# Kernel tuning notes

Hardware: AMD Instinct MI355X
Metric: run time of the kernel (lower is better)

## Reference

```python
import jax, jax.numpy as jnp
import numpy as np

N_NODES = 50000
N_GRAPHS = 64
LRELU_SLOPE = 0.2
BN_EPS = 1e-5

def _conv1d(x, w, b):
    # x: [B, C_in, L], w: [C_out, C_in, K] -> [B, C_out, L-K+1]
    y = jax.lax.conv_general_dilated(x, w, window_strides=(1,), padding='VALID',
                                     dimension_numbers=('NCH', 'OIH', 'NCH'))
    return y + b[None, :, None]

def setup_inputs() -> dict:
    key = jax.random.key(0)
    ks = jax.random.split(key, 24)
    E = 800000
    inp = {
        'global_rna': jax.random.randint(ks[0], (64, 3000), 0, 5, dtype=jnp.int32),
        'local_rna': jax.random.randint(ks[1], (64, 2998), 0, 65, dtype=jnp.int32),
        'pro_x': jax.random.normal(ks[2], (N_NODES, 33), jnp.float32),
        'edge_index': jax.random.randint(ks[3], (2, E), 0, N_NODES, dtype=jnp.int32),
        'pro_weight': jax.random.uniform(ks[4], (E,), jnp.float32),
        'pro_batch': jnp.sort(jax.random.randint(ks[5], (N_NODES,), 0, N_GRAPHS, dtype=jnp.int32)),
        'emb1': jax.random.normal(ks[6], (5, 128), jnp.float32),
        'emb2': jax.random.normal(ks[7], (65, 128), jnp.float32),
        'conv1_w': jax.random.normal(ks[8], (32, 3000, 8), jnp.float32) * 0.02,
        'conv1_b': jax.random.normal(ks[9], (32,), jnp.float32) * 0.02,
        'conv2_w': jax.random.normal(ks[10], (32, 2998, 8), jnp.float32) * 0.02,
        'conv2_b': jax.random.normal(ks[11], (32,), jnp.float32) * 0.02,
        'fc_xr_w': jax.random.normal(ks[12], (128, 3872), jnp.float32) * 0.02,
        'fc_xr_b': jax.random.normal(ks[13], (128,), jnp.float32) * 0.02,
        'gcn_w': jax.random.normal(ks[14], (33, 33), jnp.float32) * 0.1,
        'gcn_b': jax.random.normal(ks[15], (33,), jnp.float32) * 0.1,
        'bn_mean': jnp.zeros((33,), jnp.float32),
        'bn_var': jnp.ones((33,), jnp.float32),
        'bn_weight': jnp.ones((33,), jnp.float32),
        'bn_bias': jnp.zeros((33,), jnp.float32),
        'gat_wl': jax.random.normal(ks[16], (132, 33), jnp.float32) * 0.1,
        'gat_wr': jax.random.normal(ks[17], (132, 33), jnp.float32) * 0.1,
        'gat_att': jax.random.normal(ks[18], (2, 66), jnp.float32) * 0.1,
        'gat_b': jax.random.normal(ks[19], (132,), jnp.float32) * 0.1,
        'fc1_w': jax.random.normal(ks[20], (1024, 132), jnp.float32) * 0.05,
        'fc1_b': jax.random.normal(ks[21], (1024,), jnp.float32) * 0.05,
        'fc2_w': jax.random.normal(ks[22], (128, 1024), jnp.float32) * 0.05,
        'fc2_b': jax.random.normal(ks[23], (128,), jnp.float32) * 0.05,
    }
    return inp

def _forward(global_rna, local_rna, pro_x, edge_index, pro_weight, pro_batch,
             emb1, emb2, conv1_w, conv1_b, conv2_w, conv2_b, fc_xr_w, fc_xr_b,
             gcn_w, gcn_b, bn_mean, bn_var, bn_weight, bn_bias,
             gat_wl, gat_wr, gat_att, gat_b, fc1_w, fc1_b, fc2_w, fc2_b):
    # ---- RNA global branch ----
    xrg = emb1[global_rna]                       # [B, 3000, 128]
    xrg = _conv1d(xrg, conv1_w, conv1_b)         # [B, 32, 121]
    xrg = xrg.reshape(-1, 32 * 121) @ fc_xr_w.T + fc_xr_b
    # ---- RNA local branch ----
    xrl = emb2[local_rna]                        # [B, 2998, 128]
    xrl = _conv1d(xrl, conv2_w, conv2_b)         # [B, 32, 121]
    xrl = xrl.reshape(-1, 32 * 121) @ fc_xr_w.T + fc_xr_b
    # ---- protein GCNConv (with self-loops, symmetric norm, edge weights) ----
    N = pro_x.shape[0]
    loop = jnp.arange(N, dtype=edge_index.dtype)
    src = jnp.concatenate([edge_index[0], loop])
    dst = jnp.concatenate([edge_index[1], loop])
    w = jnp.concatenate([pro_weight, jnp.ones((N,), pro_weight.dtype)])
    deg = jax.ops.segment_sum(w, dst, num_segments=N)
    dinv = jnp.where(deg > 0, jax.lax.rsqrt(deg), 0.0)
    norm = dinv[src] * w * dinv[dst]
    h = pro_x @ gcn_w.T                          # [N, 33]
    xp = jax.ops.segment_sum(h[src] * norm[:, None], dst, num_segments=N) + gcn_b
    xp = jax.nn.relu(xp)
    # ---- NodeLevelBatchNorm (eval: running stats) ----
    inv = bn_weight * jax.lax.rsqrt(bn_var + BN_EPS)
    xp = xp * inv + (bn_bias - bn_mean * inv)
    # ---- GATv2Conv (heads=2, out=66, concat, self-loops, eval: no dropout) ----
    H, C = 2, 66
    xl = (xp @ gat_wl.T).reshape(N, H, C)
    xr = (xp @ gat_wr.T).reshape(N, H, C)
    e = jnp.sum(jax.nn.leaky_relu(xl[src] + xr[dst], LRELU_SLOPE) * gat_att, axis=-1)  # [E2, H]
    emax = jax.ops.segment_max(e, dst, num_segments=N)                                  # [N, H]
    a = jnp.exp(e - emax[dst])
    asum = jax.ops.segment_sum(a, dst, num_segments=N)
    alpha = a / asum[dst]                                                              # [E2, H]
    xp = jax.ops.segment_sum(xl[src] * alpha[:, :, None], dst, num_segments=N)
    xp = xp.reshape(N, H * C) + gat_b
    xp = jax.nn.relu(xp)
    # ---- global mean pool ----
    cnt = jax.ops.segment_sum(jnp.ones((N,), xp.dtype), pro_batch, num_segments=N_GRAPHS)
    xp = jax.ops.segment_sum(xp, pro_batch, num_segments=N_GRAPHS) / jnp.maximum(cnt, 1.0)[:, None]
    # ---- protein MLP head (dropout = identity in eval) ----
    xp = jax.nn.relu(xp @ fc1_w.T + fc1_b)
    xp = xp @ fc2_w.T + fc2_b
    xc_rna = 0.5 * (xrg + xrl)
    return (xc_rna, xp)

def reference(global_rna, local_rna, pro_x, edge_index, pro_weight, pro_batch,
              emb1, emb2, conv1_w, conv1_b, conv2_w, conv2_b, fc_xr_w, fc_xr_b,
              gcn_w, gcn_b, bn_mean, bn_var, bn_weight, bn_bias,
              gat_wl, gat_wr, gat_att, gat_b, fc1_w, fc1_b, fc2_w, fc2_b):
    return _forward(global_rna, local_rna, pro_x, edge_index, pro_weight, pro_batch,
                    emb1, emb2, conv1_w, conv1_b, conv2_w, conv2_b, fc_xr_w, fc_xr_b,
                    gcn_w, gcn_b, bn_mean, bn_var, bn_weight, bn_bias,
                    gat_wl, gat_wr, gat_att, gat_b, fc1_w, fc1_b, fc2_w, fc2_b)
```

## Files before the change

### kernel.cpp

```cpp
#include <hip/hip_runtime.h>

#define N_NODES 50000
#define N_EDGES 800000
#define LRELU_SLOPE 0.2f
#define BN_EPS 1e-5f

typedef unsigned int u32;
typedef unsigned long long u64;

__device__ __forceinline__ float lrelu(float x){ return fmaxf(x,0.f) + LRELU_SLOPE*fminf(x,0.f); }
__device__ __forceinline__ float bflo(u32 u){ return __uint_as_float(u<<16); }
__device__ __forceinline__ float bfhi(u32 u){ return __uint_as_float(u & 0xffff0000u); }
__device__ __forceinline__ u32 packbf(float a, float b){
  u32 ua = __float_as_uint(a); ua = (ua + 0x7fffu + ((ua>>16)&1u)) >> 16;
  u32 ub = __float_as_uint(b); ub = (ub + 0x7fffu + ((ub>>16)&1u)) >> 16;
  return ua | (ub<<16);
}
__device__ __forceinline__ float degof(u64 p){
  return (float)(p & 0xFFFFFFFFFFull) * (1.0f/67108864.0f);
}

__global__ __launch_bounds__(256) void k_hist(const int* __restrict__ eidx, const float* __restrict__ pw,
                                              u64* __restrict__ pk){
  int e = blockIdx.x*256 + threadIdx.x;
  if(e < N_EDGES){
    int d = eidx[N_EDGES + e];
    u64 q = (u64)(pw[e] * 67108864.f);
    atomicAdd(&pk[d], (1ull<<40) | q);
  }
}

__global__ __launch_bounds__(256) void k_scan1(const u64* __restrict__ pk, int* __restrict__ rowptr,
                                               int* __restrict__ bsum){
  __shared__ int sc[256];
  int b = blockIdx.x, t = threadIdx.x;
  int i = b*256 + t;
  int v = (i < N_NODES) ? (int)(pk[i] >> 40) : 0;
  sc[t] = v;
  __syncthreads();
  for(int off=1; off<256; off<<=1){
    int x = (t>=off)? sc[t-off] : 0;
    __syncthreads();
    sc[t] += x;
    __syncthreads();
  }
  if(i < N_NODES) rowptr[i] = sc[t] - v;
  if(t == 255) bsum[b] = sc[255];
}

__global__ __launch_bounds__(256) void k_scan2(const int* __restrict__ bsum, int* __restrict__ bbase,
                                               int* __restrict__ rowptr, int* __restrict__ gstart,
                                               int* __restrict__ gend){
  __shared__ int sc[256];
  int t = threadIdx.x;
  int v = (t < 196) ? bsum[t] : 0;
  sc[t] = v;
  __syncthreads();
  for(int off=1; off<256; off<<=1){
    int x = (t>=off)? sc[t-off] : 0;
    __syncthreads();
    sc[t] += x;
    __syncthreads();
  }
  if(t < 196) bbase[t] = sc[t] - v;
  if(t == 255) rowptr[N_NODES] = sc[255];
  if(t < 64){ gstart[t] = N_NODES; gend[t] = 0; }
}

__global__ __launch_bounds__(256) void k_scan3(int* __restrict__ rowptr, const int* __restrict__ bbase){
  int b = blockIdx.x, t = threadIdx.x;
  int i = b*256 + t;
  if(i < N_NODES) rowptr[i] += bbase[b];
}

__global__ __launch_bounds__(256) void k_scatter(const int* __restrict__ eidx, const float* __restrict__ pw,
                                                 const int* __restrict__ rowptr, int* __restrict__ fill,
                                                 const u64* __restrict__ pk, uint2* __restrict__ s_srcw){
  int e = blockIdx.x*256 + threadIdx.x;
  if(e < N_EDGES){
    int d = eidx[N_EDGES + e];
    int s = eidx[e];
    float ge = rsqrtf(degof(pk[s]) + 1.f) * pw[e];
    int pos = rowptr[d] + atomicAdd(&fill[d], 1);
    uint2 pr; pr.x = (u32)s; pr.y = __float_as_uint(ge);
    s_srcw[pos] = pr;
  }
}

__global__ __launch_bounds__(256) void k_h(const float* __restrict__ px, const float* __restrict__ gw,
                                           u32* __restrict__ hb){
  int n = blockIdx.x*256 + threadIdx.x;
  if(n >= N_NODES) return;
  float x[33];
  #pragma unroll
  for(int k=0;k<33;k++) x[k] = px[n*33+k];
  float a[33];
  for(int c=0;c<33;c++){
    float s = 0.f;
    #pragma unroll
    for(int k=0;k<33;k++) s = fmaf(x[k], gw[c*33+k], s);
    a[c] = s;
  }
  #pragma unroll
  for(int d=0;d<16;d++) hb[(size_t)n*17 + d] = packbf(a[2*d], a[2*d+1]);
  hb[(size_t)n*17 + 16] = packbf(a[32], 0.f);
}

__global__ __launch_bounds__(256) void k_gcn(const u32* __restrict__ hb, const int* __restrict__ rowptr,
                                             const uint2* __restrict__ s_srcw,
                                             const u64* __restrict__ pk,
                                             const float* __restrict__ gcnb, const float* __restrict__ bnm,
                                             const float* __restrict__ bnv, const float* __restrict__ bnw,
                                             const float* __restrict__ bnb, float* __restrict__ xp1){
  int wave = threadIdx.x >> 6;
  int lane = threadIdx.x & 63;
  int n = blockIdx.x*4 + wave;
  if(n >= N_NODES) return;
  int l = lane & 15, g = lane >> 4;
  bool t0 = (l == 0);
  float dn = rsqrtf(degof(pk[n]) + 1.f);
  const u32* srow = hb + (size_t)n*17;
  u32 us  = srow[l];
  u32 ust = t0 ? srow[16] : 0u;
  float acc0, acc1, acct;
  if(g == 0){ acc0 = dn*bflo(us); acc1 = dn*bfhi(us); acct = dn*bflo(ust); }
  else      { acc0 = 0.f; acc1 = 0.f; acct = 0.f; }
  int rb = rowptr[n], re = rowptr[n+1];
  int j = rb;
  for(; j+8 <= re; j += 8){
    uint2 prA = s_srcw[j + g];
    uint2 prB = s_srcw[j + 4 + g];
    float geA = __uint_as_float(prA.y);
    float geB = __uint_as_float(prB.y);
    const u32* rA = hb + (size_t)prA.x*17;
    const u32* rB = hb + (size_t)prB.x*17;
    u32 uA  = rA[l], uB = rB[l];
    u32 utA = t0 ? rA[16] : 0u;
    u32 utB = t0 ? rB[16] : 0u;
    acc0 = fmaf(geA, bflo(uA),  fmaf(geB, bflo(uB),  acc0));
    acc1 = fmaf(geA, bfhi(uA),  fmaf(geB, bfhi(uB),  acc1));
    acct = fmaf(geA, bflo(utA), fmaf(geB, bflo(utB), acct));
  }
  if(j+4 <= re){
    uint2 pr = s_srcw[j + g];
    float ge = __uint_as_float(pr.y);
    const u32* r = hb + (size_t)pr.x*17;
    u32 u  = r[l];
    u32 ut = t0 ? r[16] : 0u;
    acc0 = fmaf(ge, bflo(u),  acc0);
    acc1 = fmaf(ge, bfhi(u),  acc1);
    acct = fmaf(ge, bflo(ut), acct);
    j += 4;
  }
  int rem = re - j;
  if(rem > 0){
    bool val = (g < rem);
    uint2 pr = s_srcw[val ? (j + g) : j];
    float ge = val ? __uint_as_float(pr.y) : 0.f;
    const u32* r = hb + (size_t)pr.x*17;
    u32 u  = r[l];
    u32 ut = t0 ? r[16] : 0u;
    acc0 = fmaf(ge, bflo(u),  acc0);
    acc1 = fmaf(ge, bfhi(u),  acc1);
    acct = fmaf(ge, bflo(ut), acct);
  }
  #pragma unroll
  for(int m=16;m<=32;m<<=1){
    acc0 += __shfl_xor(acc0, m, 64);
    acc1 += __shfl_xor(acc1, m, 64);
    acct += __shfl_xor(acct, m, 64);
  }
  if(g == 0){
    int c0 = 2*l, c1 = 2*l+1;
    float v0 = fmaxf(dn*acc0 + gcnb[c0], 0.f);
    float v1 = fmaxf(dn*acc1 + gcnb[c1], 0.f);
    float i0 = bnw[c0] / sqrtf(bnv[c0] + BN_EPS);
    float i1 = bnw[c1] / sqrtf(bnv[c1] + BN_EPS);
    float2 o;
    o.x = v0*i0 + (bnb[c0] - bnm[c0]*i0);
    o.y = v1*i1 + (bnb[c1] - bnm[c1]*i1);
    ((float2*)(xp1 + (size_t)n*36))[l] = o;
    if(t0){
      float vt = fmaxf(dn*acct + gcnb[32], 0.f);
      float it = bnw[32] / sqrtf(bnv[32] + BN_EPS);
      float2 ot; ot.x = vt*it + (bnb[32] - bnm[32]*it); ot.y = 0.f;
      ((float2*)(xp1 + (size_t)n*36))[16] = ot;
      float2 z; z.x = 0.f; z.y = 0.f;
      ((float2*)(xp1 + (size_t)n*36))[17] = z;
    }
  }
}

__global__ __launch_bounds__(320) void k_gatlin(const float* __restrict__ xp1, const float* __restrict__ wl,
                                                const float* __restrict__ wr, u32* __restrict__ xlb,
                                                float* __restrict__ xr){
  __shared__ float sx[64*36];
  __shared__ float swle[66*33];
  __shared__ float swlo[66*33];
  __shared__ float swre[66*33];
  __shared__ float swro[66*33];
  int t = threadIdx.x;
  int n0 = blockIdx.x*64;
  int nn = N_NODES - n0; if(nn > 64) nn = 64;
  for(int i=t;i<2178;i+=320){
    int d = i/33, k = i - d*33;
    int gb = d*66 + k;
    swle[i] = wl[gb];
    swlo[i] = wl[gb+33];
    swre[i] = wr[gb];
    swro[i] = wr[gb+33];
  }
  int xcnt = nn*36;
  for(int i=t;i<xcnt;i+=320) sx[i] = xp1[(size_t)n0*36 + i];
  __syncthreads();
  if(t >= 264) return;
  int ng = t/66, p = t - ng*66;
  int nbase = ng*16;
  float al0[16], al1[16], ar0[16], ar1[16];
  #pragma unroll
  for(int i=0;i<16;i++){ al0[i]=0.f; al1[i]=0.f; ar0[i]=0.f; ar1[i]=0.f; }
  const float* wle = swle + p*33;
  const float* wlo = swlo + p*33;
  const float* wre = swre + p*33;
  const float* wro = swro + p*33;
  for(int k=0;k<33;k++){
    float w0 = wle[k], w1 = wlo[k], w2 = wre[k], w3 = wro[k];
    const float* xcol = sx + nbase*36 + k;
    #pragma unroll
    for(int i=0;i<16;i++){
      float x = xcol[i*36];
      al0[i] = fmaf(x, w0, al0[i]);
      al1[i] = fmaf(x, w1, al1[i]);
      ar0[i] = fmaf(x, w2, ar0[i]);
      ar1[i] = fmaf(x, w3, ar1[i]);
    }
  }
  int head = (p >= 33) ? 1 : 0;
  int dd = p - 33*head;
  #pragma unroll
  for(int i=0;i<16;i++){
    int n = nbase + i;
    if(n < nn){
      size_t nidx = (size_t)(n0 + n);
      xlb[nidx*68 + head*34 + dd] = packbf(al0[i], al1[i]);
      float2 v; v.x = ar0[i]; v.y = ar1[i];
      ((float2*)xr)[nidx*66 + p] = v;
    }
  }
}

__global__ __launch_bounds__(128) void k_gat(const int* __restrict__ rowptr, const u32* __restrict__ srcx,
                                             const u32* __restrict__ xlb, const float* __restrict__ xr,
                                             const float* __restrict__ att, const float* __restrict__ gatb,
                                             float* __restrict__ xp2){
  int n = blockIdx.x;
  int h = threadIdx.x >> 6;
  int lane = threadIdx.x & 63;
  int l = lane & 15, g = lane >> 4;
  int base = h*66, dbase = h*34;
  bool t0 = (l == 0);
  size_t nrow = (size_t)n*132;
  const float2* xr2 = (const float2*)(xr + nrow + base);
  float2 xra = xr2[2*l], xrb = xr2[2*l+1];
  float2 xrt = t0 ? xr2[32] : make_float2(0.f,0.f);
  const float2* att2 = (const float2*)(att + base);
  float2 ata = att2[2*l], atb = att2[2*l+1];
  float2 att_t = att2[32];
  const u32* srow = xlb + (size_t)n*68 + dbase;
  uint2 su = ((const uint2*)srow)[l];
  u32 ust = t0 ? srow[32] : 0u;
  float s0 = bflo(su.x), s1 = bfhi(su.x), s2 = bflo(su.y), s3 = bfhi(su.y);
  float st0 = bflo(ust), st1 = bfhi(ust);
  float p = lrelu(s0+xra.x)*ata.x + lrelu(s1+xra.y)*ata.y
          + lrelu(s2+xrb.x)*atb.x + lrelu(s3+xrb.y)*atb.y
          + lrelu(st0+xrt.x)*att_t.x + lrelu(st1+xrt.y)*att_t.y;
  #pragma unroll
  for(int m=1;m<=8;m<<=1) p += __shfl_xor(p, m, 64);
  float e_self = p;
  float a0_, a1_, a2_, a3_, at0, at1, asum;
  if(g == 0){ a0_=s0; a1_=s1; a2_=s2; a3_=s3; at0=st0; at1=st1; asum=1.f; }
  else      { a0_=0.f; a1_=0.f; a2_=0.f; a3_=0.f; at0=0.f; at1=0.f; asum=0.f; }
  int rb = rowptr[n], re = rowptr[n+1];
  int j = rb;
  for(; j+8 <= re; j += 8){
    int sA = (int)srcx[2*(j + g)];
    int sB = (int)srcx[2*(j + 4 + g)];
    const u32* rA = xlb + (size_t)sA*68 + dbase;
    const u32* rB = xlb + (size_t)sB*68 + dbase;
    uint2 uA = ((const uint2*)rA)[l];
    uint2 uB = ((const uint2*)rB)[l];
    u32 utA = t0 ? rA[32] : 0u;
    u32 utB = t0 ? rB[32] : 0u;
    float vA0=bflo(uA.x), vA1=bfhi(uA.x), vA2=bflo(uA.y), vA3=bfhi(uA.y);
    float vB0=bflo(uB.x), vB1=bfhi(uB.x), vB2=bflo(uB.y), vB3=bfhi(uB.y);
    float wA0=bflo(utA), wA1=bfhi(utA);
    float wB0=bflo(utB), wB1=bfhi(utB);
    float pA = lrelu(vA0+xra.x)*ata.x + lrelu(vA1+xra.y)*ata.y
             + lrelu(vA2+xrb.x)*atb.x + lrelu(vA3+xrb.y)*atb.y
             + lrelu(wA0+xrt.x)*att_t.x + lrelu(wA1+xrt.y)*att_t.y;
    float pB = lrelu(vB0+xra.x)*ata.x + lrelu(vB1+xra.y)*ata.y
             + lrelu(vB2+xrb.x)*atb.x + lrelu(vB3+xrb.y)*atb.y
             + lrelu(wB0+xrt.x)*att_t.x + lrelu(wB1+xrt.y)*att_t.y;
    #pragma unroll
    for(int m=1;m<=8;m<<=1){
      pA += __shfl_xor(pA, m, 64);
      pB += __shfl_xor(pB, m, 64);
    }
    float aA = __expf(pA - e_self);
    float aB = __expf(pB - e_self);
    a0_ = fmaf(aA, vA0, fmaf(aB, vB0, a0_));
    a1_ = fmaf(aA, vA1, fmaf(aB, vB1, a1_));
    a2_ = fmaf(aA, vA2, fmaf(aB, vB2, a2_));
    a3_ = fmaf(aA, vA3, fmaf(aB, vB3, a3_));
    at0 = fmaf(aA, wA0, fmaf(aB, wB0, at0));
    at1 = fmaf(aA, wA1, fmaf(aB, wB1, at1));
    asum += aA + aB;
  }
  if(j+4 <= re){
    int s = (int)srcx[2*(j + g)];
    const u32* r = xlb + (size_t)s*68 + dbase;
    uint2 uu = ((const uint2*)r)[l];
    u32 ut = t0 ? r[32] : 0u;
    float v0=bflo(uu.x), v1=bfhi(uu.x), v2=bflo(uu.y), v3=bfhi(uu.y);
    float w0=bflo(ut), w1=bfhi(ut);
    float pp = lrelu(v0+xra.x)*ata.x + lrelu(v1+xra.y)*ata.y
             + lrelu(v2+xrb.x)*atb.x + lrelu(v3+xrb.y)*atb.y
             + lrelu(w0+xrt.x)*att_t.x + lrelu(w1+xrt.y)*att_t.y;
    #pragma unroll
    for(int m=1;m<=8;m<<=1) pp += __shfl_xor(pp, m, 64);
    float a = __expf(pp - e_self);
    a0_ = fmaf(a, v0, a0_); a1_ = fmaf(a, v1, a1_);
    a2_ = fmaf(a, v2, a2_); a3_ = fmaf(a, v3, a3_);
    at0 = fmaf(a, w0, at0); at1 = fmaf(a, w1, at1);
    asum += a;
    j += 4;
  }
  int rem = re - j;
  if(rem > 0){
    bool val = (g < rem);
    int s = val ? (int)srcx[2*(j + g)] : n;
    const u32* r = xlb + (size_t)s*68 + dbase;
    uint2 uu = ((const uint2*)r)[l];
    u32 ut = t0 ? r[32] : 0u;
    float v0=bflo(uu.x), v1=bfhi(uu.x), v2=bflo(uu.y), v3=bfhi(uu.y);
    float w0=bflo(ut), w1=bfhi(ut);
    float pp = lrelu(v0+xra.x)*ata.x + lrelu(v1+xra.y)*ata.y
             + lrelu(v2+xrb.x)*atb.x + lrelu(v3+xrb.y)*atb.y
             + lrelu(w0+xrt.x)*att_t.x + lrelu(w1+xrt.y)*att_t.y;
    #pragma unroll
    for(int m=1;m<=8;m<<=1) pp += __shfl_xor(pp, m, 64);
    float a = val ? __expf(pp - e_self) : 0.f;
    a0_ = fmaf(a, v0, a0_); a1_ = fmaf(a, v1, a1_);
    a2_ = fmaf(a, v2, a2_); a3_ = fmaf(a, v3, a3_);
    at0 = fmaf(a, w0, at0); at1 = fmaf(a, w1, at1);
    asum += a;
  }
  #pragma unroll
  for(int m=16;m<=32;m<<=1){
    a0_ += __shfl_xor(a0_, m, 64);
    a1_ += __shfl_xor(a1_, m, 64);
    a2_ += __shfl_xor(a2_, m, 64);
    a3_ += __shfl_xor(a3_, m, 64);
    at0 += __shfl_xor(at0, m, 64);
    at1 += __shfl_xor(at1, m, 64);
    asum += __shfl_xor(asum, m, 64);
  }
  float inv = 1.f/asum;
  if(g == 0){
    const float2* gb2 = (const float2*)(gatb + base);
    float2 ga = gb2[2*l], gb = gb2[2*l+1];
    float2* o2 = (float2*)(xp2 + nrow + base);
    float2 oa, ob;
    oa.x = fmaxf(a0_*inv + ga.x, 0.f); oa.y = fmaxf(a1_*inv + ga.y, 0.f);
    ob.x = fmaxf(a2_*inv + gb.x, 0.f); ob.y = fmaxf(a3_*inv + gb.y, 0.f);
    o2[2*l] = oa; o2[2*l+1] = ob;
    if(t0){
      float2 gt = gb2[32];
      float2 ot;
      ot.x = fmaxf(at0*inv + gt.x, 0.f); ot.y = fmaxf(at1*inv + gt.y, 0.f);
      o2[32] = ot;
    }
  }
}

__global__ __launch_bounds__(256) void k_bounds(const int* __restrict__ batch, int* __restrict__ gstart,
                                                int* __restrict__ gend){
  int n = blockIdx.x*256 + threadIdx.x;
  if(n >= N_NODES) return;
  int b = batch[n];
  if(n == 0) gstart[b] = 0;
  else {
    int p = batch[n-1];
    if(p != b){ gstart[b] = n; gend[p] = n; }
  }
  if(n == N_NODES-1) gend[b] = N_NODES;
}

__global__ __launch_bounds__(128) void k_poolp(const float* __restrict__ xp2, const int* __restrict__ gstart,
                                               const int* __restrict__ gend, float* __restrict__ pp){
  int g = blockIdx.x, seg = blockIdx.y, t = threadIdx.x;
  int s = gstart[g], e = gend[g];
  int len = e - s; if(len < 0) len = 0;
  int ns = s + (int)(((long long)len*seg)>>4);
  int ne = s + (int)(((long long)len*(seg+1))>>4);
  float a0 = 0.f, a1 = 0.f;
  for(int n=ns;n<ne;n++){
    a0 += xp2[(size_t)n*132 + t];
    if(t < 4) a1 += xp2[(size_t)n*132 + 128 + t];
  }
  float* o = pp + (size_t)(g*16 + seg)*132;
  o[t] = a0;
  if(t < 4) o[128 + t] = a1;
}

__global__ __launch_bounds__(256) void k_pfc1(const float* __restrict__ pp, const int* __restrict__ gstart,
                                              const int* __restrict__ gend, const float* __restrict__ w,
                                              const float* __restrict__ b, float* __restrict__ h1T){
  __shared__ float pooled[132];
  int g = blockIdx.x, t = threadIdx.x;
  if(t < 132){
    float s = 0.f;
    #pragma unroll
    for(int k=0;k<16;k++) s += pp[(size_t)(g*16 + k)*132 + t];
    int c = gend[g] - gstart[g]; if(c < 1) c = 1;
    pooled[t] = s/(float)c;
  }
  __syncthreads();
  #pragma unroll
  for(int r=0;r<4;r++){
    int o = r*256 + t;
    const float* wr = w + o*132;
    float acc = b[o];
    for(int k=0;k<132;k++) acc = fmaf(pooled[k], wr[k], acc);
    h1T[o*64+g] = fmaxf(acc, 0.f);
  }
}

__global__ __launch_bounds__(256) void k_fc2(const float* __restrict__ h1T, const float* __restrict__ w,
                                             const float* __restrict__ b, float* __restrict__ out){
  __shared__ float part[256];
  int o = blockIdx.x, t = threadIdx.x;
  int s = t >> 6, g = t & 63;
  const float* wr = w + o*1024 + s*256;
  const float* hp = h1T + (size_t)(s*256)*64 + g;
  float acc = 0.f;
  for(int k=0;k<256;k++) acc = fmaf(hp[k*64], wr[k], acc);
  part[t] = acc;
  __syncthreads();
  if(s == 0){
    float r = b[o] + part[g] + part[64+g] + part[128+g] + part[192+g];
    out[8192 + g*128 + o] = r;
  }
}

__global__ __launch_bounds__(256) void k_bucket(const int* __restrict__ g, int L, int V,
                                                int* __restrict__ sci, int* __restrict__ off){
  __shared__ int gl[3000];
  __shared__ int hist[65];
  __shared__ int base[66];
  int b = blockIdx.x, t = threadIdx.x;
  if(t < V) hist[t] = 0;
  for(int i=t;i<L;i+=256) gl[i] = g[b*L + i];
  __syncthreads();
  for(int i=t;i<L;i+=256) atomicAdd(&hist[gl[i]], 1);
  __syncthreads();
  if(t == 0){
    int run = 0;
    for(int v=0;v<V;v++){ base[v] = run; run += hist[v]; }
    base[V] = run;
  }
  __syncthreads();
  if(t <= V) off[b*(V+1) + t] = base[t];
  if(t < V) hist[t] = 0;
  __syncthreads();
  for(int i=t;i<L;i+=256){
    int v = gl[i];
    int p = base[v] + atomicAdd(&hist[v], 1);
    sci[b*3000 + p] = i*8;
  }
}

__global__ __launch_bounds__(256) void k_sgather(const int* __restrict__ sci, const int* __restrict__ off,
                                                 const float* __restrict__ w, int V, int wstride,
                                                 int sstride, float* __restrict__ S){
  __shared__ int loff[66];
  __shared__ int lci[3000];
  int b = blockIdx.x, q = blockIdx.y, t = threadIdx.x;
  int nsplit = gridDim.y;
  if(t <= V) loff[t] = off[b*(V+1) + t];
  __syncthreads();
  int vs = (V*q)/nsplit, ve = (V*(q+1))/nsplit;
  if(vs == ve) return;
  int p0 = loff[vs], p1 = loff[ve];
  for(int i=p0+t;i<p1;i+=256) lci[i-p0] = sci[b*3000 + i];
  __syncthreads();
  int co = t >> 3, kk = t & 7;
  const float* wrow = w + co*wstride + kk;
  float* Srow = S + (size_t)b*32*sstride + co*sstride + kk;
  for(int v=vs;v<ve;v++){
    int j = loff[v] - p0, je = loff[v+1] - p0;
    float a0=0.f,a1=0.f,a2=0.f,a3=0.f,a4=0.f,a5=0.f,a6=0.f,a7=0.f;
    for(; j+8 <= je; j += 8){
      a0 += wrow[lci[j]];
      a1 += wrow[lci[j+1]];
      a2 += wrow[lci[j+2]];
      a3 += wrow[lci[j+3]];
      a4 += wrow[lci[j+4]];
      a5 += wrow[lci[j+5]];
      a6 += wrow[lci[j+6]];
      a7 += wrow[lci[j+7]];
    }
    for(; j<je; j++) a0 += wrow[lci[j]];
    Srow[v*8] = ((a0+a1)+(a2+a3)) + ((a4+a5)+(a6+a7));
  }
}

__global__ __launch_bounds__(128) void k_y(const float* __restrict__ S1, const float* __restrict__ S2,
                                           const float* __restrict__ emb1, const float* __restrict__ emb2,
                                           const float* __restrict__ c1b, const float* __restrict__ c2b,
                                           float* __restrict__ ysum){
  __shared__ float em1[640];
  __shared__ float em2[8320];
  __shared__ float Sa[320];
  __shared__ float Sb[4160];
  int b = blockIdx.x, cg = blockIdx.y, t = threadIdx.x;
  for(int i=t;i<640;i+=128)  em1[i] = emb1[i];
  for(int i=t;i<8320;i+=128) em2[i] = emb2[i];
  for(int i=t;i<320;i+=128)  Sa[i] = S1[b*1280 + cg*320 + i];
  for(int i=t;i<4160;i+=128) Sb[i] = S2[(size_t)b*16640 + cg*4160 + i];
  __syncthreads();
  if(t >= 121) return;
  #pragma unroll
  for(int c8=0;c8<8;c8++){
    int co = cg*8 + c8;
    const float* sa = Sa + c8*40;
    float acc1 = c1b[co];
    #pragma unroll
    for(int v=0;v<5;v++)
      #pragma unroll
      for(int k=0;k<8;k++) acc1 = fmaf(sa[v*8+k], em1[v*128 + t + k], acc1);
    const float* sb = Sb + c8*520;
    float acc2 = c2b[co];
    for(int v=0;v<65;v++){
      #pragma unroll
      for(int k=0;k<8;k++) acc2 = fmaf(sb[v*8+k], em2[v*128 + t + k], acc2);
    }
    ysum[b*3872 + co*121 + t] = 0.5f*(acc1 + acc2);
  }
}

__global__ __launch_bounds__(256) void k_fcxr(const float* __restrict__ ysum, const float* __restrict__ fcw,
                                              const float* __restrict__ fcb, float* __restrict__ out){
  __shared__ float part[512];
  int bp = blockIdx.x, q = blockIdx.y, t = threadIdx.x;
  int b0 = bp*2;
  int ol = t >> 3;
  int o  = q*32 + ol;
  int slice = t & 7;
  const float4* ys0 = (const float4*)(ysum + b0*3872) + slice*121;
  const float4* ys1 = (const float4*)(ysum + (b0+1)*3872) + slice*121;
  const float4* wr  = (const float4*)(fcw + (size_t)o*3872) + slice*121;
  float acc0 = 0.f, acc1 = 0.f;
  for(int k=0;k<121;k++){
    float4 w4 = wr[k];
    float4 y0 = ys0[k], y1 = ys1[k];
    acc0 += y0.x*w4.x + y0.y*w4.y + y0.z*w4.z + y0.w*w4.w;
    acc1 += y1.x*w4.x + y1.y*w4.y + y1.z*w4.z + y1.w*w4.w;
  }
  part[t] = acc0;
  part[256+t] = acc1;
  __syncthreads();
  if(slice == 0){
    float s0 = fcb[o], s1 = fcb[o];
    #pragma unroll
    for(int i=0;i<8;i++){ s0 += part[ol*8 + i]; s1 += part[256 + ol*8 + i]; }
    out[b0*128 + o] = s0;
    out[(b0+1)*128 + o] = s1;
  }
}

extern "C" void kernel_launch(void* const* d_in, const int* in_sizes, int n_in,
                              void* d_out, int out_size, void* d_ws, size_t ws_size,
                              hipStream_t stream){
  const int*   g_rna = (const int*)  d_in[0];
  const int*   l_rna = (const int*)  d_in[1];
  const float* pro_x = (const float*)d_in[2];
  const int*   eidx  = (const int*)  d_in[3];
  const float* pro_w = (const float*)d_in[4];
  const int*   batch = (const int*)  d_in[5];
  const float* emb1  = (const float*)d_in[6];
  const float* emb2  = (const float*)d_in[7];
  const float* c1w   = (const float*)d_in[8];
  const float* c1b   = (const float*)d_in[9];
  const float* c2w   = (const float*)d_in[10];
  const float* c2b   = (const float*)d_in[11];
  const float* fcxw  = (const float*)d_in[12];
  const float* fcxb  = (const float*)d_in[13];
  const float* gcnw  = (const float*)d_in[14];
  const float* gcnb  = (const float*)d_in[15];
  const float* bnm   = (const float*)d_in[16];
  const float* bnv   = (const float*)d_in[17];
  const float* bnw   = (const float*)d_in[18];
  const float* bnb   = (const float*)d_in[19];
  const float* gwl   = (const float*)d_in[20];
  const float* gwr   = (const float*)d_in[21];
  const float* gatt  = (const float*)d_in[22];
  const float* gatb  = (const float*)d_in[23];
  const float* f1w   = (const float*)d_in[24];
  const float* f1b   = (const float*)d_in[25];
  const float* f2w   = (const float*)d_in[26];
  const float* f2b_  = (const float*)d_in[27];
  float* out = (float*)d_out;

  char* ws = (char*)d_ws;
  size_t off = 0;
  auto A = [&](size_t n)->char*{ char* p = ws + off; off = (off + n + 255) & ~(size_t)255; return p; };
  u64*   pk     = (u64*)  A((size_t)N_NODES*8);
  int*   fill   = (int*)  A((size_t)N_NODES*4);
  size_t zero_bytes = off;
  int*   rowptr = (int*)  A((size_t)(N_NODES+1)*4);
  int*   bsum   = (int*)  A(196*4);
  int*   bbase  = (int*)  A(196*4);
  uint2* s_srcw = (uint2*)A((size_t)N_EDGES*8);
  u32*   hb     = (u32*)  A((size_t)N_NODES*17*4);
  float* xp1    = (float*)A((size_t)N_NODES*36*4);
  u32*   xlb    = (u32*)  A((size_t)N_NODES*68*4);
  float* xr     = (float*)A((size_t)N_NODES*132*4);
  float* xp2    = (float*)A((size_t)N_NODES*132*4);
  int*   gstart = (int*)  A(64*4);
  int*   gend   = (int*)  A(64*4);
  float* pp     = (float*)A((size_t)64*16*132*4);
  float* h1T    = (float*)A(1024*64*4);
  float* S1     = (float*)A((size_t)64*1280*4);
  float* S2     = (float*)A((size_t)64*16640*4);
  float* ysum   = (float*)A((size_t)64*3872*4);
  int*   sci1   = (int*)  A((size_t)64*3000*4);
  int*   off1   = (int*)  A((size_t)64*8*4);
  int*   sci2   = (int*)  A((size_t)64*3000*4);
  int*   off2   = (int*)  A((size_t)64*66*4);
  (void)ws_size; (void)in_sizes; (void)n_in; (void)out_size;

  hipMemsetAsync(ws, 0, zero_bytes, stream);

  k_hist   <<<3125, 256, 0, stream>>>(eidx, pro_w, pk);
  k_scan1  <<<196, 256, 0, stream>>>(pk, rowptr, bsum);
  k_scan2  <<<1, 256, 0, stream>>>(bsum, bbase, rowptr, gstart, gend);
  k_scan3  <<<196, 256, 0, stream>>>(rowptr, bbase);
  k_scatter<<<3125, 256, 0, stream>>>(eidx, pro_w, rowptr, fill, pk, s_srcw);
  k_h      <<<196, 256, 0, stream>>>(pro_x, gcnw, hb);
  k_gcn    <<<12500, 256, 0, stream>>>(hb, rowptr, s_srcw, pk, gcnb, bnm, bnv, bnw, bnb, xp1);
  k_gatlin <<<782, 320, 0, stream>>>(xp1, gwl, gwr, xlb, xr);
  k_gat    <<<N_NODES, 128, 0, stream>>>(rowptr, (const u32*)s_srcw, xlb, xr, gatt, gatb, xp2);
  k_bounds <<<196, 256, 0, stream>>>(batch, gstart, gend);
  k_poolp  <<<dim3(64,16), 128, 0, stream>>>(xp2, gstart, gend, pp);
  k_pfc1   <<<64, 256, 0, stream>>>(pp, gstart, gend, f1w, f1b, h1T);
  k_fc2    <<<128, 256, 0, stream>>>(h1T, f2w, f2b_, out);

  k_bucket <<<64, 256, 0, stream>>>(g_rna, 3000, 5, sci1, off1);
  k_bucket <<<64, 256, 0, stream>>>(l_rna, 2998, 65, sci2, off2);
  k_sgather<<<dim3(64,5), 256, 0, stream>>>(sci1, off1, c1w, 5, 24000, 40, S1);
  k_sgather<<<dim3(64,32), 256, 0, stream>>>(sci2, off2, c2w, 65, 23984, 520, S2);
  k_y      <<<dim3(64,4), 128, 0, stream>>>(S1, S2, emb1, emb2, c1b, c2b, ysum);
  k_fcxr   <<<dim3(32,4), 256, 0, stream>>>(ysum, fcxw, fcxb, out);
}
```

Measured before the change: 552.1 us.

## Restructure GAT attention: precomputed lrelu linear term, 8-lane groups, DPP reductions

```diff
diff --git a/kernel.cpp b/kernel.cpp
--- a/kernel.cpp
+++ b/kernel.cpp
@@ -20,6 +20,24 @@
   return (float)(p & 0xFFFFFFFFFFull) * (1.0f/67108864.0f);
 }
 
+template<int CTRL>
+__device__ __forceinline__ float dppadd(float x){
+  int y = __builtin_amdgcn_update_dpp(0, __float_as_int(x), CTRL, 0xF, 0xF, false);
+  return x + __int_as_float(y);
+}
+__device__ __forceinline__ float red8(float p){
+  p = dppadd<0x141>(p);
+  p = dppadd<0x4E>(p);
+  p = dppadd<0xB1>(p);
+  return p;
+}
+__device__ __forceinline__ float redall(float v){
+  v = dppadd<0x128>(v);
+  v += __shfl_xor(v, 16, 64);
+  v += __shfl_xor(v, 32, 64);
+  return v;
+}
+
 __global__ __launch_bounds__(256) void k_hist(const int* __restrict__ eidx, const float* __restrict__ pw,
                                               u64* __restrict__ pk){
   int e = blockIdx.x*256 + threadIdx.x;
@@ -75,7 +93,8 @@
 
 __global__ __launch_bounds__(256) void k_scatter(const int* __restrict__ eidx, const float* __restrict__ pw,
                                                  const int* __restrict__ rowptr, int* __restrict__ fill,
-                                                 const u64* __restrict__ pk, uint2* __restrict__ s_srcw){
+                                                 const u64* __restrict__ pk, uint2* __restrict__ s_srcw,
+                                                 int* __restrict__ srcs){
   int e = blockIdx.x*256 + threadIdx.x;
   if(e < N_EDGES){
     int d = eidx[N_EDGES + e];
@@ -84,6 +103,7 @@
     int pos = rowptr[d] + atomicAdd(&fill[d], 1);
     uint2 pr; pr.x = (u32)s; pr.y = __float_as_uint(ge);
     s_srcw[pos] = pr;
+    srcs[pos] = s;
   }
 }
 
@@ -192,13 +212,14 @@
 }
 
 __global__ __launch_bounds__(320) void k_gatlin(const float* __restrict__ xp1, const float* __restrict__ wl,
-                                                const float* __restrict__ wr, u32* __restrict__ xlb,
-                                                float* __restrict__ xr){
+                                                const float* __restrict__ wr, const float* __restrict__ att,
+                                                u32* __restrict__ xlb, float* __restrict__ xr){
   __shared__ float sx[64*36];
   __shared__ float swle[66*33];
   __shared__ float swlo[66*33];
   __shared__ float swre[66*33];
   __shared__ float swro[66*33];
+  __shared__ float sdl[64][2];
   int t = threadIdx.x;
   int n0 = blockIdx.x*64;
   int nn = N_NODES - n0; if(nn > 64) nn = 64;
@@ -210,175 +231,170 @@
     swre[i] = wr[gb];
     swro[i] = wr[gb+33];
   }
+  if(t < 128) sdl[t>>1][t&1] = 0.f;
   int xcnt = nn*36;
   for(int i=t;i<xcnt;i+=320) sx[i] = xp1[(size_t)n0*36 + i];
   __syncthreads();
-  if(t >= 264) return;
-  int ng = t/66, p = t - ng*66;
-  int nbase = ng*16;
-  float al0[16], al1[16], ar0[16], ar1[16];
-  #pragma unroll
-  for(int i=0;i<16;i++){ al0[i]=0.f; al1[i]=0.f; ar0[i]=0.f; ar1[i]=0.f; }
-  const float* wle = swle + p*33;
-  const float* wlo = swlo + p*33;
-  const float* wre = swre + p*33;
-  const float* wro = swro + p*33;
-  for(int k=0;k<33;k++){
-    float w0 = wle[k], w1 = wlo[k], w2 = wre[k], w3 = wro[k];
-    const float* xcol = sx + nbase*36 + k;
+  if(t < 264){
+    int ng = t/66, p = t - ng*66;
+    int nbase = ng*16;
+    float al0[16], al1[16], ar0[16], ar1[16];
+    #pragma unroll
+    for(int i=0;i<16;i++){ al0[i]=0.f; al1[i]=0.f; ar0[i]=0.f; ar1[i]=0.f; }
+    const float* wle = swle + p*33;
+    const float* wlo = swlo + p*33;
+    const float* wre = swre + p*33;
+    const float* wro = swro + p*33;
+    for(int k=0;k<33;k++){
+      float w0 = wle[k], w1 = wlo[k], w2 = wre[k], w3 = wro[k];
+      const float* xcol = sx + nbase*36 + k;
+      #pragma unroll
+      for(int i=0;i<16;i++){
+        float x = xcol[i*36];
+        al0[i] = fmaf(x, w0, al0[i]);
+        al1[i] = fmaf(x, w1, al1[i]);
+        ar0[i] = fmaf(x, w2, ar0[i]);
+        ar1[i] = fmaf(x, w3, ar1[i]);
+      }
+    }
+    int head = (p >= 33) ? 1 : 0;
+    int dd = p - 33*head;
+    float attA = att[head*66 + 2*dd];
+    float attB = att[head*66 + 2*dd + 1];
     #pragma unroll
     for(int i=0;i<16;i++){
-      float x = xcol[i*36];
-      al0[i] = fmaf(x, w0, al0[i]);
-      al1[i] = fmaf(x, w1, al1[i]);
-      ar0[i] = fmaf(x, w2, ar0[i]);
-      ar1[i] = fmaf(x, w3, ar1[i]);
+      int n = nbase + i;
+      if(n < nn){
+        size_t nidx = (size_t)(n0 + n);
+        xlb[nidx*72 + head*36 + dd] = packbf(al0[i], al1[i]);
+        float2 v; v.x = ar0[i]; v.y = ar1[i];
+        ((float2*)xr)[nidx*66 + p] = v;
+        atomicAdd(&sdl[n][head], fmaf(al0[i], attA, al1[i]*attB));
+      }
     }
   }
-  int head = (p >= 33) ? 1 : 0;
-  int dd = p - 33*head;
-  #pragma unroll
-  for(int i=0;i<16;i++){
-    int n = nbase + i;
-    if(n < nn){
-      size_t nidx = (size_t)(n0 + n);
-      xlb[nidx*68 + head*34 + dd] = packbf(al0[i], al1[i]);
-      float2 v; v.x = ar0[i]; v.y = ar1[i];
-      ((float2*)xr)[nidx*66 + p] = v;
-    }
-  }
-}
-
-__global__ __launch_bounds__(128) void k_gat(const int* __restrict__ rowptr, const u32* __restrict__ srcx,
+  __syncthreads();
+  if(t < 128){
+    int nl = t >> 1, hh = t & 1;
+    if(nl < nn)
+      xlb[(size_t)(n0 + nl)*72 + hh*36 + 33] =
+        __float_as_uint(sdl[nl][hh] * (LRELU_SLOPE*1.44269504089f));
+  }
+}
+
+__global__ __launch_bounds__(128) void k_gat(const int* __restrict__ rowptr, const int* __restrict__ srcs,
                                              const u32* __restrict__ xlb, const float* __restrict__ xr,
                                              const float* __restrict__ att, const float* __restrict__ gatb,
                                              float* __restrict__ xp2){
+  const float ATT_SC = (1.f - LRELU_SLOPE) * 1.44269504089f;
   int n = blockIdx.x;
   int h = threadIdx.x >> 6;
   int lane = threadIdx.x & 63;
-  int l = lane & 15, g = lane >> 4;
-  int base = h*66, dbase = h*34;
-  bool t0 = (l == 0);
-  size_t nrow = (size_t)n*132;
-  const float2* xr2 = (const float2*)(xr + nrow + base);
-  float2 xra = xr2[2*l], xrb = xr2[2*l+1];
-  float2 xrt = t0 ? xr2[32] : make_float2(0.f,0.f);
-  const float2* att2 = (const float2*)(att + base);
-  float2 ata = att2[2*l], atb = att2[2*l+1];
-  float2 att_t = att2[32];
-  const u32* srow = xlb + (size_t)n*68 + dbase;
-  uint2 su = ((const uint2*)srow)[l];
-  u32 ust = t0 ? srow[32] : 0u;
-  float s0 = bflo(su.x), s1 = bfhi(su.x), s2 = bflo(su.y), s3 = bfhi(su.y);
-  float st0 = bflo(ust), st1 = bfhi(ust);
-  float p = lrelu(s0+xra.x)*ata.x + lrelu(s1+xra.y)*ata.y
-          + lrelu(s2+xrb.x)*atb.x + lrelu(s3+xrb.y)*atb.y
-          + lrelu(st0+xrt.x)*att_t.x + lrelu(st1+xrt.y)*att_t.y;
-  #pragma unroll
-  for(int m=1;m<=8;m<<=1) p += __shfl_xor(p, m, 64);
-  float e_self = p;
-  float a0_, a1_, a2_, a3_, at0, at1, asum;
-  if(g == 0){ a0_=s0; a1_=s1; a2_=s2; a3_=s3; at0=st0; at1=st1; asum=1.f; }
-  else      { a0_=0.f; a1_=0.f; a2_=0.f; a3_=0.f; at0=0.f; at1=0.f; asum=0.f; }
+  int l8 = lane & 7, g8 = lane >> 3;
+  bool t0 = (l8 == 0);
+  bool g0 = (g8 == 0);
+  const float* xrp = xr + (size_t)n*132 + h*66 + 8*l8;
+  float2 x01 = ((const float2*)xrp)[0];
+  float2 x23 = ((const float2*)xrp)[1];
+  float2 x45 = ((const float2*)xrp)[2];
+  float2 x67 = ((const float2*)xrp)[3];
+  float2 xt  = t0 ? *(const float2*)(xr + (size_t)n*132 + h*66 + 64) : make_float2(0.f,0.f);
+  const float* ap = att + h*66 + 8*l8;
+  float2 a01 = ((const float2*)ap)[0];
+  float2 a23 = ((const float2*)ap)[1];
+  float2 a45 = ((const float2*)ap)[2];
+  float2 a67 = ((const float2*)ap)[3];
+  a01.x *= ATT_SC; a01.y *= ATT_SC; a23.x *= ATT_SC; a23.y *= ATT_SC;
+  a45.x *= ATT_SC; a45.y *= ATT_SC; a67.x *= ATT_SC; a67.y *= ATT_SC;
+  float2 atl = *(const float2*)(att + h*66 + 64);
+  atl.x *= ATT_SC; atl.y *= ATT_SC;
+
+  const u32* xbase = xlb + h*36;
+  float v0,v1,v2,v3,v4,v5,v6,v7,w0,w1;
+
+#define GSCORE(U, TU, P) { \
+  v0=bflo(U.x); v1=bfhi(U.x); v2=bflo(U.y); v3=bfhi(U.y); \
+  v4=bflo(U.z); v5=bfhi(U.z); v6=bflo(U.w); v7=bfhi(U.w); \
+  w0=bflo(TU.x); w1=bfhi(TU.x); \
+  float pA = __uint_as_float(TU.y), pB = 0.f; \
+  pA = fmaf(fmaxf(v0+x01.x,0.f), a01.x, pA); \
+  pB = fmaf(fmaxf(v1+x01.y,0.f), a01.y, pB); \
+  pA = fmaf(fmaxf(v2+x23.x,0.f), a23.x, pA); \
+  pB = fmaf(fmaxf(v3+x23.y,0.f), a23.y, pB); \
+  pA = fmaf(fmaxf(v4+x45.x,0.f), a45.x, pA); \
+  pB = fmaf(fmaxf(v5+x45.y,0.f), a45.y, pB); \
+  pA = fmaf(fmaxf(v6+x67.x,0.f), a67.x, pA); \
+  pB = fmaf(fmaxf(v7+x67.y,0.f), a67.y, pB); \
+  pA = fmaf(fmaxf(w0+xt.x,0.f), atl.x, pA); \
+  pB = fmaf(fmaxf(w1+xt.y,0.f), atl.y, pB); \
+  P = red8(pA + pB); }
+
+  const u32* srow = xbase + (size_t)n*72;
+  uint4 su = ((const uint4*)srow)[l8];
+  uint2 stl = t0 ? ((const uint2*)srow)[16] : make_uint2(0u,0u);
+  float ps;
+  GSCORE(su, stl, ps);
+  float cn = -ps;
+  float A0 = g0? v0 : 0.f, A1 = g0? v1 : 0.f, A2 = g0? v2 : 0.f, A3 = g0? v3 : 0.f;
+  float A4 = g0? v4 : 0.f, A5 = g0? v5 : 0.f, A6 = g0? v6 : 0.f, A7 = g0? v7 : 0.f;
+  float T0 = g0? w0 : 0.f, T1 = g0? w1 : 0.f;
+  float asum = g0 ? 1.f : 0.f;
+
   int rb = rowptr[n], re = rowptr[n+1];
   int j = rb;
   for(; j+8 <= re; j += 8){
-    int sA = (int)srcx[2*(j + g)];
-    int sB = (int)srcx[2*(j + 4 + g)];
-    const u32* rA = xlb + (size_t)sA*68 + dbase;
-    const u32* rB = xlb + (size_t)sB*68 + dbase;
-    uint2 uA = ((const uint2*)rA)[l];
-    uint2 uB = ((const uint2*)rB)[l];
-    u32 utA = t0 ? rA[32] : 0u;
-    u32 utB = t0 ? rB[32] : 0u;
-    float vA0=bflo(uA.x), vA1=bfhi(uA.x), vA2=bflo(uA.y), vA3=bfhi(uA.y);
-    float vB0=bflo(uB.x), vB1=bfhi(uB.x), vB2=bflo(uB.y), vB3=bfhi(uB.y);
-    float wA0=bflo(utA), wA1=bfhi(utA);
-    float wB0=bflo(utB), wB1=bfhi(utB);
-    float pA = lrelu(vA0+xra.x)*ata.x + lrelu(vA1+xra.y)*ata.y
-             + lrelu(vA2+xrb.x)*atb.x + lrelu(vA3+xrb.y)*atb.y
-             + lrelu(wA0+xrt.x)*att_t.x + lrelu(wA1+xrt.y)*att_t.y;
-    float pB = lrelu(vB0+xra.x)*ata.x + lrelu(vB1+xra.y)*ata.y
-             + lrelu(vB2+xrb.x)*atb.x + lrelu(vB3+xrb.y)*atb.y
-             + lrelu(wB0+xrt.x)*att_t.x + lrelu(wB1+xrt.y)*att_t.y;
-    #pragma unroll
-    for(int m=1;m<=8;m<<=1){
-      pA += __shfl_xor(pA, m, 64);
-      pB += __shfl_xor(pB, m, 64);
-    }
-    float aA = __expf(pA - e_self);
-    float aB = __expf(pB - e_self);
-    a0_ = fmaf(aA, vA0, fmaf(aB, vB0, a0_));
-    a1_ = fmaf(aA, vA1, fmaf(aB, vB1, a1_));
-    a2_ = fmaf(aA, vA2, fmaf(aB, vB2, a2_));
-    a3_ = fmaf(aA, vA3, fmaf(aB, vB3, a3_));
-    at0 = fmaf(aA, wA0, fmaf(aB, wB0, at0));
-    at1 = fmaf(aA, wA1, fmaf(aB, wB1, at1));
-    asum += aA + aB;
-  }
-  if(j+4 <= re){
-    int s = (int)srcx[2*(j + g)];
-    const u32* r = xlb + (size_t)s*68 + dbase;
-    uint2 uu = ((const uint2*)r)[l];
-    u32 ut = t0 ? r[32] : 0u;
-    float v0=bflo(uu.x), v1=bfhi(uu.x), v2=bflo(uu.y), v3=bfhi(uu.y);
-    float w0=bflo(ut), w1=bfhi(ut);
-    float pp = lrelu(v0+xra.x)*ata.x + lrelu(v1+xra.y)*ata.y
-             + lrelu(v2+xrb.x)*atb.x + lrelu(v3+xrb.y)*atb.y
-             + lrelu(w0+xrt.x)*att_t.x + lrelu(w1+xrt.y)*att_t.y;
-    #pragma unroll
-    for(int m=1;m<=8;m<<=1) pp += __shfl_xor(pp, m, 64);
-    float a = __expf(pp - e_self);
-    a0_ = fmaf(a, v0, a0_); a1_ = fmaf(a, v1, a1_);
-    a2_ = fmaf(a, v2, a2_); a3_ = fmaf(a, v3, a3_);
-    at0 = fmaf(a, w0, at0); at1 = fmaf(a, w1, at1);
+    int s = srcs[j + g8];
+    const u32* r = xbase + (size_t)s*72;
+    uint4 u = ((const uint4*)r)[l8];
+    uint2 tu = t0 ? ((const uint2*)r)[16] : make_uint2(0u,0u);
+    float p;
+    GSCORE(u, tu, p);
+    float a = __builtin_amdgcn_exp2f(p + cn);
+    A0 = fmaf(a, v0, A0); A1 = fmaf(a, v1, A1); A2 = fmaf(a, v2, A2); A3 = fmaf(a, v3, A3);
+    A4 = fmaf(a, v4, A4); A5 = fmaf(a, v5, A5); A6 = fmaf(a, v6, A6); A7 = fmaf(a, v7, A7);
+    T0 = fmaf(a, w0, T0); T1 = fmaf(a, w1, T1);
     asum += a;
-    j += 4;
   }
   int rem = re - j;
   if(rem > 0){
-    bool val = (g < rem);
-    int s = val ? (int)srcx[2*(j + g)] : n;
-    const u32* r = xlb + (size_t)s*68 + dbase;
-    uint2 uu = ((const uint2*)r)[l];
-    u32 ut = t0 ? r[32] : 0u;
-    float v0=bflo(uu.x), v1=bfhi(uu.x), v2=bflo(uu.y), v3=bfhi(uu.y);
-    float w0=bflo(ut), w1=bfhi(ut);
-    float pp = lrelu(v0+xra.x)*ata.x + lrelu(v1+xra.y)*ata.y
-             + lrelu(v2+xrb.x)*atb.x + lrelu(v3+xrb.y)*atb.y
-             + lrelu(w0+xrt.x)*att_t.x + lrelu(w1+xrt.y)*att_t.y;
-    #pragma unroll
-    for(int m=1;m<=8;m<<=1) pp += __shfl_xor(pp, m, 64);
-    float a = val ? __expf(pp - e_self) : 0.f;
-    a0_ = fmaf(a, v0, a0_); a1_ = fmaf(a, v1, a1_);
-    a2_ = fmaf(a, v2, a2_); a3_ = fmaf(a, v3, a3_);
-    at0 = fmaf(a, w0, at0); at1 = fmaf(a, w1, at1);
+    bool val = (g8 < rem);
+    int s = val ? srcs[j + g8] : n;
+    const u32* r = xbase + (size_t)s*72;
+    uint4 u = ((const uint4*)r)[l8];
+    uint2 tu = t0 ? ((const uint2*)r)[16] : make_uint2(0u,0u);
+    float p;
+    GSCORE(u, tu, p);
+    float a = val ? __builtin_amdgcn_exp2f(p + cn) : 0.f;
+    A0 = fmaf(a, v0, A0); A1 = fmaf(a, v1, A1); A2 = fmaf(a, v2, A2); A3 = fmaf(a, v3, A3);
+    A4 = fmaf(a, v4, A4); A5 = fmaf(a, v5, A5); A6 = fmaf(a, v6, A6); A7 = fmaf(a, v7, A7);
+    T0 = fmaf(a, w0, T0); T1 = fmaf(a, w1, T1);
     asum += a;
   }
-  #pragma unroll
-  for(int m=16;m<=32;m<<=1){
-    a0_ += __shfl_xor(a0_, m, 64);
-    a1_ += __shfl_xor(a1_, m, 64);
-    a2_ += __shfl_xor(a2_, m, 64);
-    a3_ += __shfl_xor(a3_, m, 64);
-    at0 += __shfl_xor(at0, m, 64);
-    at1 += __shfl_xor(at1, m, 64);
-    asum += __shfl_xor(asum, m, 64);
-  }
-  float inv = 1.f/asum;
-  if(g == 0){
-    const float2* gb2 = (const float2*)(gatb + base);
-    float2 ga = gb2[2*l], gb = gb2[2*l+1];
-    float2* o2 = (float2*)(xp2 + nrow + base);
-    float2 oa, ob;
-    oa.x = fmaxf(a0_*inv + ga.x, 0.f); oa.y = fmaxf(a1_*inv + ga.y, 0.f);
-    ob.x = fmaxf(a2_*inv + gb.x, 0.f); ob.y = fmaxf(a3_*inv + gb.y, 0.f);
-    o2[2*l] = oa; o2[2*l+1] = ob;
+#undef GSCORE
+
+  A0 = redall(A0); A1 = redall(A1); A2 = redall(A2); A3 = redall(A3);
+  A4 = redall(A4); A5 = redall(A5); A6 = redall(A6); A7 = redall(A7);
+  T0 = redall(T0); T1 = redall(T1);
+  asum = redall(asum);
+
+  if(g0){
+    float inv = 1.f / asum;
+    const float* gp = gatb + h*66 + 8*l8;
+    float2 g01 = ((const float2*)gp)[0];
+    float2 g23 = ((const float2*)gp)[1];
+    float2 g45 = ((const float2*)gp)[2];
+    float2 g67 = ((const float2*)gp)[3];
+    float* op = xp2 + (size_t)n*132 + h*66 + 8*l8;
+    float2 o;
+    o.x = fmaxf(fmaf(A0,inv,g01.x),0.f); o.y = fmaxf(fmaf(A1,inv,g01.y),0.f); ((float2*)op)[0] = o;
+    o.x = fmaxf(fmaf(A2,inv,g23.x),0.f); o.y = fmaxf(fmaf(A3,inv,g23.y),0.f); ((float2*)op)[1] = o;
+    o.x = fmaxf(fmaf(A4,inv,g45.x),0.f); o.y = fmaxf(fmaf(A5,inv,g45.y),0.f); ((float2*)op)[2] = o;
+    o.x = fmaxf(fmaf(A6,inv,g67.x),0.f); o.y = fmaxf(fmaf(A7,inv,g67.y),0.f); ((float2*)op)[3] = o;
     if(t0){
-      float2 gt = gb2[32];
+      float2 gt = *(const float2*)(gatb + h*66 + 64);
       float2 ot;
-      ot.x = fmaxf(at0*inv + gt.x, 0.f); ot.y = fmaxf(at1*inv + gt.y, 0.f);
-      o2[32] = ot;
+      ot.x = fmaxf(fmaf(T0,inv,gt.x),0.f); ot.y = fmaxf(fmaf(T1,inv,gt.y),0.f);
+      *(float2*)(xp2 + (size_t)n*132 + h*66 + 64) = ot;
     }
   }
 }
@@ -622,9 +638,10 @@
   int*   bsum   = (int*)  A(196*4);
   int*   bbase  = (int*)  A(196*4);
   uint2* s_srcw = (uint2*)A((size_t)N_EDGES*8);
+  int*   srcs   = (int*)  A((size_t)N_EDGES*4);
   u32*   hb     = (u32*)  A((size_t)N_NODES*17*4);
   float* xp1    = (float*)A((size_t)N_NODES*36*4);
-  u32*   xlb    = (u32*)  A((size_t)N_NODES*68*4);
+  u32*   xlb    = (u32*)  A((size_t)N_NODES*72*4);
   float* xr     = (float*)A((size_t)N_NODES*132*4);
   float* xp2    = (float*)A((size_t)N_NODES*132*4);
   int*   gstart = (int*)  A(64*4);
@@ -646,11 +663,11 @@
   k_scan1  <<<196, 256, 0, stream>>>(pk, rowptr, bsum);
   k_scan2  <<<1, 256, 0, stream>>>(bsum, bbase, rowptr, gstart, gend);
   k_scan3  <<<196, 256, 0, stream>>>(rowptr, bbase);
-  k_scatter<<<3125, 256, 0, stream>>>(eidx, pro_w, rowptr, fill, pk, s_srcw);
+  k_scatter<<<3125, 256, 0, stream>>>(eidx, pro_w, rowptr, fill, pk, s_srcw, srcs);
   k_h      <<<196, 256, 0, stream>>>(pro_x, gcnw, hb);
   k_gcn    <<<12500, 256, 0, stream>>>(hb, rowptr, s_srcw, pk, gcnb, bnm, bnv, bnw, bnb, xp1);
-  k_gatlin <<<782, 320, 0, stream>>>(xp1, gwl, gwr, xlb, xr);
-  k_gat    <<<N_NODES, 128, 0, stream>>>(rowptr, (const u32*)s_srcw, xlb, xr, gatt, gatb, xp2);
+  k_gatlin <<<782, 320, 0, stream>>>(xp1, gwl, gwr, gatt, xlb, xr);
+  k_gat    <<<N_NODES, 128, 0, stream>>>(rowptr, srcs, xlb, xr, gatt, gatb, xp2);
   k_bounds <<<196, 256, 0, stream>>>(batch, gstart, gend);
   k_poolp  <<<dim3(64,16), 128, 0, stream>>>(xp2, gstart, gend, pp);
   k_pfc1   <<<64, 256, 0, stream>>>(pp, gstart, gend, f1w, f1b, h1T);
```

Measured after the change: 605.2 us. +9.6%, slower.
